# Performance work log

Hardware: AMD Instinct MI355X
Metric: run time of the kernel (lower is better)

Reference implementation:

```python
import jax, jax.numpy as jnp
import numpy as np

NUM_CLASSES = 80
REG_MAX = 16
CLS_W, BOX_W, DFL_W = 1.0, 2.5, 0.5


def _make_anchors(img=640, strides=(8, 16, 32)):
    pts, strs = [], []
    for s in strides:
        n = img // s
        xs = (np.arange(n, dtype=np.float32) + 0.5) * s
        gy, gx = np.meshgrid(xs, xs, indexing='ij')
        pts.append(np.stack([gx.ravel(), gy.ravel()], axis=1))
        strs.append(np.full((n * n, 1), float(s), np.float32))
    return np.concatenate(pts, 0).astype(np.float32), np.concatenate(strs, 0)


def setup_inputs() -> dict:
    key = jax.random.key(0)
    k1, k2, k3, k4, k5 = jax.random.split(key, 5)
    B, G = 16, 20
    ap, st = _make_anchors()  # A = 8400
    A = ap.shape[0]
    cls_scores = jax.random.uniform(k1, (B, A, NUM_CLASSES), dtype=jnp.float32)
    reg_distri = jax.random.normal(k2, (B, A, 4 * (REG_MAX + 1)), dtype=jnp.float32)
    cxcy = jax.random.uniform(k3, (B, G, 2), dtype=jnp.float32) * 560.0 + 40.0
    wh = jax.random.uniform(k4, (B, G, 2), dtype=jnp.float32) * 120.0 + 20.0
    gt_boxes = jnp.concatenate([cxcy - wh * 0.5, cxcy + wh * 0.5], axis=-1)  # xyxy
    gt_labels = jax.random.randint(k5, (B, G), 0, NUM_CLASSES)
    return {"cls_scores": cls_scores, "reg_distri": reg_distri, "gt_boxes": gt_boxes,
            "anchor_points": jnp.asarray(ap), "stride_tensor": jnp.asarray(st),
            "gt_labels": gt_labels}


def _per_image(pred_cls, pred_reg, gt_boxes, gt_labels, anchor_points, stride):
    A, C = pred_cls.shape
    G = gt_boxes.shape[0]
    k = max(min(13, A // max(G, 1)), 3)
    p = jnp.clip(pred_cls, 1e-7, 1.0 - 1e-7)
    centers = (gt_boxes[:, :2] + gt_boxes[:, 2:]) * 0.5                    # [G,2]
    d = jnp.sqrt(jnp.sum((anchor_points[:, None, :] - centers[None]) ** 2, -1))  # [A,G]
    _, topk_idx = jax.lax.top_k(-d.T, k)                                    # [G,k] nearest anchors
    ax = anchor_points[topk_idx]                                            # [G,k,2]
    inside = ((ax[..., 0] >= gt_boxes[:, None, 0]) & (ax[..., 0] <= gt_boxes[:, None, 2]) &
              (ax[..., 1] >= gt_boxes[:, None, 1]) & (ax[..., 1] <= gt_boxes[:, None, 3]))
    any_in = inside.any(-1, keepdims=True)
    assign_k = jnp.where(any_in, inside, jnp.arange(k) < 3)                 # fallback: 3 nearest
    assign = jnp.zeros((G, A), bool).at[jnp.arange(G)[:, None], topk_idx].set(assign_k)
    aT = assign.T                                                           # [A,G]
    fg = aT.any(1)                                                          # [A]
    last_gt = (G - 1) - jnp.argmax(aT[:, ::-1], axis=1)
    target_box = jnp.where(fg[:, None], gt_boxes[last_gt], 0.0)             # [A,4]
    onehot = jax.nn.one_hot(gt_labels, C, dtype=p.dtype)                    # [G,C]
    target_cls = jnp.max(aT[:, :, None].astype(p.dtype) * onehot[None], axis=1)  # [A,C]
    bce = -(target_cls * jnp.log(p) + (1.0 - target_cls) * jnp.log(1.0 - p))
    num_pos = fg.sum().astype(p.dtype)
    pos_w = jnp.minimum(A / jnp.maximum(num_pos, 1.0), 50.0)
    fgf = fg.astype(p.dtype)[:, None]
    pos_loss = jnp.where(num_pos > 0,
                         jnp.sum(bce * fgf) / jnp.maximum(num_pos * C, 1.0) * pos_w, 0.0)
    neg_loss = jnp.sum(bce * (1.0 - fgf)) / jnp.maximum((A - num_pos) * C, 1.0)
    # box decode (DFL expectation) + smooth-L1 on fg anchors
    reg = jax.nn.softmax(pred_reg.reshape(A, 4, REG_MAX + 1), axis=-1)
    proj = jnp.arange(REG_MAX + 1, dtype=p.dtype)
    dist = jnp.sum(reg * proj, axis=-1)                                     # [A,4]
    s = stride[:, 0]
    pb = jnp.stack([anchor_points[:, 0] - dist[:, 0] * s,
                    anchor_points[:, 1] - dist[:, 1] * s,
                    anchor_points[:, 0] + dist[:, 2] * s,
                    anchor_points[:, 1] + dist[:, 3] * s], axis=-1)
    diff = pb - target_box
    ad = jnp.abs(diff)
    sl1 = jnp.where(ad < 1.0, 0.5 * diff * diff, ad - 0.5)
    box_loss = jnp.where(num_pos > 0,
                         jnp.sum(sl1 * fgf) / jnp.maximum(num_pos * 4.0, 1.0), 0.0)
    return pos_loss + neg_loss, box_loss


def reference(cls_scores, reg_distri, gt_boxes, anchor_points, stride_tensor, gt_labels):
    cls_l, box_l = jax.vmap(
        lambda pc, pr, gb, gl: _per_image(pc, pr, gb, gl, anchor_points, stride_tensor)
    )(cls_scores, reg_distri, gt_boxes, gt_labels)
    loss_cls = cls_l.mean() * CLS_W
    loss_box = box_l.mean() * BOX_W
    return loss_cls + loss_box  # loss_dfl is identically 0 in the original
```

## Files before the change

### kernel.cpp

```cpp
#include <hip/hip_runtime.h>
#include <hip/hip_bf16.h>
#include <cfloat>

#define C_NUM 80
#define REG_MAXP1 17
#define NS 33
#define MAXA 8448
#define FG_STRIDE 512

__device__ inline void cand_for_slot(int sc, float cx, float cy, float& v, int& idx)
{
    v = FLT_MAX; idx = 0x7fffffff;
    int loc, w, n, strd, base;
    if (sc < 36)      { loc = sc;      w = 6; n = 80; strd = 8;  base = 0; }
    else if (sc < 52) { loc = sc - 36; w = 4; n = 40; strd = 16; base = 6400; }
    else if (sc < 68) { loc = sc - 52; w = 4; n = 20; strd = 32; base = 8000; }
    else return;
    float inv = 1.0f / (float)strd;
    int ix0 = (int)floorf(cx * inv - 0.5f) - (w / 2 - 1);
    int iy0 = (int)floorf(cy * inv - 0.5f) - (w / 2 - 1);
    int ix = ix0 + loc % w, iy = iy0 + loc / w;
    if (ix < 0 || ix >= n || iy < 0 || iy >= n) return;
    float ax = ((float)ix + 0.5f) * (float)strd;
    float ay = ((float)iy + 0.5f) * (float)strd;
    float dx = ax - cx, dy = ay - cy;
    v = dx * dx + dy * dy;
    idx = base + iy * n + ix;
}

__global__ __launch_bounds__(1024) void assignraster_kernel(const float* __restrict__ gt_boxes,
                              unsigned int* __restrict__ mask,
                              int* __restrict__ fglist,
                              int* __restrict__ npos,
                              float* __restrict__ acc,
                              int A, int G, int k)
{
    __shared__ unsigned int lmask[8400];
    __shared__ int s_cnt;
    int b = blockIdx.x, t = threadIdx.x;
    int wv = t >> 6, lane = t & 63;

    for (int i = t; i < A; i += 1024) lmask[i] = 0u;
    if (t == 0) s_cnt = 0;
    if (t < 3) acc[b * 3 + t] = 0.f;
    __syncthreads();

    for (int g = wv; g < G; g += 16) {
        const float* box = gt_boxes + (size_t)(b * G + g) * 4;
        float x0 = box[0], y0 = box[1], x1 = box[2], y1 = box[3];
        float cx = (x0 + x1) * 0.5f, cy = (y0 + y1) * 0.5f;

        float v0, v1; int i0, i1;
        cand_for_slot(lane,      cx, cy, v0, i0);
        cand_for_slot(lane + 64, cx, cy, v1, i1);

        int my_sel = 0x7fffffff;
        for (int it = 0; it < k; ++it) {
            float lb; int li; bool s0;
            if (v0 < v1 || (v0 == v1 && i0 < i1)) { lb = v0; li = i0; s0 = true; }
            else                                   { lb = v1; li = i1; s0 = false; }
            float rb = lb; int ri = li;
            for (int off = 32; off; off >>= 1) {
                float ov = __shfl_down(rb, off);
                int   oi = __shfl_down(ri, off);
                if (ov < rb || (ov == rb && oi < ri)) { rb = ov; ri = oi; }
            }
            int win = __shfl(ri, 0);
            if (lane == it) my_sel = win;
            if (li == win) {
                if (s0) { v0 = FLT_MAX; i0 = 0x7fffffff; }
                else    { v1 = FLT_MAX; i1 = 0x7fffffff; }
            }
        }

        bool inside = false;
        if (lane < k && my_sel < 0x7fffffff) {
            int idx = my_sel, n, strd, base;
            if (idx < 6400)      { n = 80; strd = 8;  base = 0; }
            else if (idx < 8000) { n = 40; strd = 16; base = 6400; }
            else                 { n = 20; strd = 32; base = 8000; }
            int loc = idx - base;
            float ax = ((float)(loc % n) + 0.5f) * (float)strd;
            float ay = ((float)(loc / n) + 0.5f) * (float)strd;
            inside = (ax >= x0) && (ax <= x1) && (ay >= y0) && (ay <= y1);
        }
        unsigned long long ball = __ballot(inside);
        if (lane < k && my_sel < 0x7fffffff) {
            bool asg = ball ? inside : (lane < 3);
            if (asg) atomicOr(&lmask[my_sel], 1u << g);
        }
    }
    __syncthreads();

    for (int i = t; i < A; i += 1024) {
        unsigned int m = lmask[i];
        mask[(size_t)b * A + i] = m;
        bool fg = (m != 0u);
        unsigned long long bal = __ballot(fg);
        int cnt = __popcll(bal);
        int base = 0;
        if (lane == 0 && cnt) base = atomicAdd(&s_cnt, cnt);
        base = __shfl(base, 0);
        if (fg) {
            int pre = __popcll(bal & ((1ull << lane) - 1ull));
            fglist[b * FG_STRIDE + base + pre] = i | ((31 - __clz(m)) << 16);
        }
    }
    __syncthreads();
    if (t == 0) npos[b] = s_cnt;
}

__global__ __launch_bounds__(256) void assign_kernel(const float* __restrict__ gt_boxes,
                              const float* __restrict__ anchor_points,
                              int* __restrict__ sel,
                              int B, int A, int G, int k)
{
    __shared__ float s_val[4];
    __shared__ int   s_idx[4];
    __shared__ int   s_sel;
    __shared__ int   s_topk[16];
    __shared__ int   s_anyin;

    int bg = blockIdx.x;
    int b = bg / G, g = bg % G;
    const float* box = gt_boxes + (size_t)(b * G + g) * 4;
    float x0 = box[0], y0 = box[1], x1 = box[2], y1 = box[3];
    float cx = (x0 + x1) * 0.5f, cy = (y0 + y1) * 0.5f;

    int t = threadIdx.x;
    float dv[NS];
#pragma unroll
    for (int s = 0; s < NS; ++s) {
        int i = t + s * 256;
        float d = FLT_MAX;
        if (i < A) {
            float dx = anchor_points[2 * i] - cx;
            float dy = anchor_points[2 * i + 1] - cy;
            d = dx * dx + dy * dy;
        }
        dv[s] = d;
    }

    int wid = t >> 6, lane = t & 63;
    for (int it = 0; it < k; ++it) {
        float best = FLT_MAX; int bi = 0x7fffffff;
#pragma unroll
        for (int s = 0; s < NS; ++s) {
            if (dv[s] < best) { best = dv[s]; bi = t + s * 256; }
        }
        for (int off = 32; off; off >>= 1) {
            float ov = __shfl_down(best, off);
            int   oi = __shfl_down(bi, off);
            if (ov < best || (ov == best && oi < bi)) { best = ov; bi = oi; }
        }
        if (lane == 0) { s_val[wid] = best; s_idx[wid] = bi; }
        __syncthreads();
        if (t == 0) {
            float bv = s_val[0]; int bix = s_idx[0];
#pragma unroll
            for (int w = 1; w < 4; ++w) {
                if (s_val[w] < bv || (s_val[w] == bv && s_idx[w] < bix)) { bv = s_val[w]; bix = s_idx[w]; }
            }
            s_sel = bix;
            s_topk[it] = bix;
        }
        __syncthreads();
        int selx = s_sel;
        if ((selx & 255) == t) {
            int slot = selx >> 8;
#pragma unroll
            for (int s = 0; s < NS; ++s) if (s == slot) dv[s] = FLT_MAX;
        }
    }

    if (t == 0) s_anyin = 0;
    __syncthreads();
    bool inside = false; int aidx = -1;
    if (t < k) {
        aidx = s_topk[t];
        float ax = anchor_points[2 * aidx], ay = anchor_points[2 * aidx + 1];
        inside = (ax >= x0) && (ax <= x1) && (ay >= y0) && (ay <= y1);
        if (inside) atomicOr(&s_anyin, 1);
    }
    __syncthreads();
    if (t < k) {
        bool asg = s_anyin ? inside : (t < 3);
        sel[(size_t)bg * 16 + t] = asg ? aidx : -1;
    }
}

__global__ __launch_bounds__(256) void raster_kernel(const int* __restrict__ sel,
                              unsigned int* __restrict__ mask,
                              int* __restrict__ fglist,
                              int* __restrict__ npos,
                              float* __restrict__ acc,
                              int A, int G, int k)
{
    __shared__ unsigned int lmask[MAXA];
    __shared__ int s_cnt;
    int b = blockIdx.x, t = threadIdx.x;

    for (int i = t; i < A; i += 256) lmask[i] = 0u;
    if (t == 0) s_cnt = 0;
    if (t < 3) acc[b * 3 + t] = 0.f;
    __syncthreads();

    for (int i = t; i < G * 16; i += 256) {
        int slot = i & 15;
        if (slot < k) {
            int a = sel[(size_t)(b * G) * 16 + i];
            if (a >= 0) atomicOr(&lmask[a], 1u << (i >> 4));
        }
    }
    __syncthreads();

    for (int i = t; i < A; i += 256) {
        unsigned int m = lmask[i];
        mask[(size_t)b * A + i] = m;
        if (m) {
            int lg = 31 - __clz(m);
            int p = atomicAdd(&s_cnt, 1);
            fglist[b * FG_STRIDE + p] = i | (lg << 16);
        }
    }
    __syncthreads();
    if (t == 0) npos[b] = s_cnt;
}

__device__ inline void bce4(float4 v, unsigned int m, const int* __restrict__ lab,
                            int c0, float& pos, float& neg)
{
    float p0 = fminf(fmaxf(v.x, 1e-7f), 1.0f - 1e-7f);
    float p1 = fminf(fmaxf(v.y, 1e-7f), 1.0f - 1e-7f);
    float p2 = fminf(fmaxf(v.z, 1e-7f), 1.0f - 1e-7f);
    float p3 = fminf(fmaxf(v.w, 1e-7f), 1.0f - 1e-7f);
    if (m) {
        unsigned int tm = 0, mm = m;
        while (mm) {
            int g = __ffs(mm) - 1;
            mm &= mm - 1;
            unsigned int d = (unsigned int)(lab[g] - c0);
            if (d < 4u) tm |= 1u << d;
        }
        pos -= __logf((tm & 1u) ? p0 : 1.0f - p0);
        pos -= __logf((tm & 2u) ? p1 : 1.0f - p1);
        pos -= __logf((tm & 4u) ? p2 : 1.0f - p2);
        pos -= __logf((tm & 8u) ? p3 : 1.0f - p3);
    } else {
        neg -= __logf(1.0f - p0) + __logf(1.0f - p1) + __logf(1.0f - p2) + __logf(1.0f - p3);
    }
}

__global__ __launch_bounds__(256) void cls_kernel(const float4* __restrict__ cls,
                           const unsigned int* __restrict__ mask,
                           const int* __restrict__ gt_labels,
                           float* __restrict__ acc, int A, int G)
{
    const int CQ = C_NUM / 4;
    int b = blockIdx.y;
    int nq = A * CQ;
    const float4* base = cls + (size_t)b * nq;
    const unsigned int* mrow = mask + (size_t)b * A;
    const int* lab = gt_labels + (size_t)b * G;
    int stride = gridDim.x * 256;

    float pos = 0.f, neg = 0.f;
    for (int q0 = blockIdx.x * 256 + threadIdx.x; q0 < nq; q0 += 2 * stride) {
        int q1 = q0 + stride;
        bool h1 = q1 < nq;
        float4 va = base[q0];
        unsigned int ma = mrow[q0 / CQ];
        float4 vb; unsigned int mb = 0;
        if (h1) { vb = base[q1]; mb = mrow[q1 / CQ]; }
        bce4(va, ma, lab, (q0 % CQ) * 4, pos, neg);
        if (h1) bce4(vb, mb, lab, (q1 % CQ) * 4, pos, neg);
    }

    for (int off = 32; off; off >>= 1) {
        pos += __shfl_down(pos, off);
        neg += __shfl_down(neg, off);
    }
    __shared__ float sp[4], sn[4];
    int wid = threadIdx.x >> 6, lane = threadIdx.x & 63;
    if (lane == 0) { sp[wid] = pos; sn[wid] = neg; }
    __syncthreads();
    if (threadIdx.x == 0) {
        float P = sp[0] + sp[1] + sp[2] + sp[3];
        float N = sn[0] + sn[1] + sn[2] + sn[3];
        if (P != 0.f) atomicAdd(&acc[b * 3 + 0], P);
        if (N != 0.f) atomicAdd(&acc[b * 3 + 1], N);
    }
}

__global__ __launch_bounds__(256) void boxfg_kernel(const float* __restrict__ reg,
                           const float* __restrict__ gt_boxes,
                           const float* __restrict__ ap,
                           const float* __restrict__ st,
                           const int* __restrict__ fglist,
                           const int* __restrict__ npos,
                           float* __restrict__ acc, int A, int G)
{
    int b = blockIdx.y;
    int idx = blockIdx.x * 256 + threadIdx.x;
    int e = idx >> 2, j = idx & 3;
    float bx = 0.f;
    if (e < npos[b]) {
        int ent = fglist[b * FG_STRIDE + e];
        int a = ent & 0xffff;
        int lg = ent >> 16;
        float tbj = gt_boxes[(size_t)(b * G + lg) * 4 + j];
        const float* rj = reg + ((size_t)b * A + a) * (4 * REG_MAXP1) + j * REG_MAXP1;
        float rr[REG_MAXP1];
#pragma unroll
        for (int i = 0; i < REG_MAXP1; ++i) rr[i] = rj[i];
        float mx = rr[0];
#pragma unroll
        for (int i = 1; i < REG_MAXP1; ++i) mx = fmaxf(mx, rr[i]);
        float sum = 0.f, dot = 0.f;
#pragma unroll
        for (int i = 0; i < REG_MAXP1; ++i) {
            float ev = __expf(rr[i] - mx);
            sum += ev; dot += ev * (float)i;
        }
        float dist = dot / sum;
        float s = st[a];
        float ac = ap[2 * a + (j & 1)];
        float pbj = (j < 2) ? (ac - dist * s) : (ac + dist * s);
        float df = pbj - tbj;
        float ad = fabsf(df);
        bx = (ad < 1.0f) ? 0.5f * df * df : ad - 0.5f;
    }
    for (int off = 32; off; off >>= 1) bx += __shfl_down(bx, off);
    __shared__ float sb[4];
    int wid = threadIdx.x >> 6, lane = threadIdx.x & 63;
    if (lane == 0) sb[wid] = bx;
    __syncthreads();
    if (threadIdx.x == 0) {
        float X = sb[0] + sb[1] + sb[2] + sb[3];
        if (X != 0.f) atomicAdd(&acc[b * 3 + 2], X);
    }
}

__global__ void final_kernel(const float* __restrict__ acc,
                             const int* __restrict__ npos,
                             float* __restrict__ out, int B, int A)
{
    if (threadIdx.x == 0 && blockIdx.x == 0) {
        float cls_sum = 0.f, box_sum = 0.f;
        for (int b = 0; b < B; ++b) {
            float np = (float)npos[b];
            float neg = acc[b * 3 + 1] / fmaxf(((float)A - np) * (float)C_NUM, 1.0f);
            float pos = 0.f, box = 0.f;
            if (np > 0.f) {
                float pw = fminf((float)A / fmaxf(np, 1.0f), 50.0f);
                pos = acc[b * 3 + 0] / fmaxf(np * (float)C_NUM, 1.0f) * pw;
                box = acc[b * 3 + 2] / fmaxf(np * 4.0f, 1.0f);
            }
            cls_sum += pos + neg;
            box_sum += box;
        }
        out[0] = cls_sum / (float)B * 1.0f + box_sum / (float)B * 2.5f;
    }
}

extern "C" void kernel_launch(void* const* d_in, const int* in_sizes, int n_in,
                              void* d_out, int out_size, void* d_ws, size_t ws_size,
                              hipStream_t stream)
{
    const float* cls   = (const float*)d_in[0];
    const float* reg   = (const float*)d_in[1];
    const float* gtb   = (const float*)d_in[2];
    const float* ap    = (const float*)d_in[3];
    const float* st    = (const float*)d_in[4];
    const int*   glab  = (const int*)d_in[5];

    int A = in_sizes[3] / 2;
    int B = in_sizes[0] / (A * C_NUM);
    int G = in_sizes[5] / B;
    int k = A / (G > 1 ? G : 1); if (k > 13) k = 13; if (k < 3) k = 3;

    unsigned int* mask = (unsigned int*)d_ws;
    float* acc   = (float*)(mask + (size_t)B * A);
    int*   npos  = (int*)(acc + 3 * B);
    int*   sel   = npos + B;
    int*   fgl   = sel + (size_t)B * G * 16;

    if (A == 8400 && G <= 32) {
        assignraster_kernel<<<B, 1024, 0, stream>>>(gtb, mask, fgl, npos, acc, A, G, k);
    } else {
        assign_kernel<<<B * G, 256, 0, stream>>>(gtb, ap, sel, B, A, G, k);
        raster_kernel<<<B, 256, 0, stream>>>(sel, mask, fgl, npos, acc, A, G, k);
    }

    dim3 g3(128, B);
    cls_kernel<<<g3, 256, 0, stream>>>((const float4*)cls, mask, glab, acc, A, G);

    dim3 g4((FG_STRIDE * 4 + 255) / 256, B);
    boxfg_kernel<<<g4, 256, 0, stream>>>(reg, gtb, ap, st, fgl, npos, acc, A, G);

    final_kernel<<<1, 64, 0, stream>>>(acc, npos, (float*)d_out, B, A);
}
```

Baseline: 154.8 us.

## Stream negative BCE unconditionally and fix up foreground anchors in fused kernel

The classification pass now computes the negative BCE term for every element without reading the assignment mask. A separate kernel then subtracts the negative term and adds the positive term for foreground anchors only, and also computes the box loss. The final reduction runs in the last block to finish, using a global counter, which removes the separate final kernel launch. This trades branch-free streaming for an extra correction pass and float cancellation when subtracting terms.

```diff
diff --git a/kernel.cpp b/kernel.cpp
--- a/kernel.cpp
+++ b/kernel.cpp
@@ -3,10 +3,13 @@
 #include <cfloat>
 
 #define C_NUM 80
+#define CQ 20
 #define REG_MAXP1 17
 #define NS 33
 #define MAXA 8448
 #define FG_STRIDE 512
+#define FIX_SLOTS (FG_STRIDE * CQ)
+#define FG_BLOCKS 48
 
 __device__ inline void cand_for_slot(int sc, float cx, float cy, float& v, int& idx)
 {
@@ -33,6 +36,7 @@
                               int* __restrict__ fglist,
                               int* __restrict__ npos,
                               float* __restrict__ acc,
+                              unsigned int* __restrict__ counter,
                               int A, int G, int k)
 {
     __shared__ unsigned int lmask[8400];
@@ -43,6 +47,7 @@
     for (int i = t; i < A; i += 1024) lmask[i] = 0u;
     if (t == 0) s_cnt = 0;
     if (t < 3) acc[b * 3 + t] = 0.f;
+    if (b == 0 && t == 0) *counter = 0u;
     __syncthreads();
 
     for (int g = wv; g < G; g += 16) {
@@ -194,6 +199,7 @@
                               int* __restrict__ fglist,
                               int* __restrict__ npos,
                               float* __restrict__ acc,
+                              unsigned int* __restrict__ counter,
                               int A, int G, int k)
 {
     __shared__ unsigned int lmask[MAXA];
@@ -203,6 +209,7 @@
     for (int i = t; i < A; i += 256) lmask[i] = 0u;
     if (t == 0) s_cnt = 0;
     if (t < 3) acc[b * 3 + t] = 0.f;
+    if (b == 0 && t == 0) *counter = 0u;
     __syncthreads();
 
     for (int i = t; i < G * 16; i += 256) {
@@ -227,139 +234,158 @@
     if (t == 0) npos[b] = s_cnt;
 }
 
-__device__ inline void bce4(float4 v, unsigned int m, const int* __restrict__ lab,
-                            int c0, float& pos, float& neg)
-{
-    float p0 = fminf(fmaxf(v.x, 1e-7f), 1.0f - 1e-7f);
-    float p1 = fminf(fmaxf(v.y, 1e-7f), 1.0f - 1e-7f);
-    float p2 = fminf(fmaxf(v.z, 1e-7f), 1.0f - 1e-7f);
-    float p3 = fminf(fmaxf(v.w, 1e-7f), 1.0f - 1e-7f);
-    if (m) {
-        unsigned int tm = 0, mm = m;
-        while (mm) {
-            int g = __ffs(mm) - 1;
-            mm &= mm - 1;
-            unsigned int d = (unsigned int)(lab[g] - c0);
-            if (d < 4u) tm |= 1u << d;
-        }
-        pos -= __logf((tm & 1u) ? p0 : 1.0f - p0);
-        pos -= __logf((tm & 2u) ? p1 : 1.0f - p1);
-        pos -= __logf((tm & 4u) ? p2 : 1.0f - p2);
-        pos -= __logf((tm & 8u) ? p3 : 1.0f - p3);
-    } else {
+__global__ __launch_bounds__(256) void cls_stream_kernel(const float4* __restrict__ cls,
+                           float* __restrict__ acc, int nq)
+{
+    int b = blockIdx.y;
+    const float4* base = cls + (size_t)b * nq;
+    int stride = gridDim.x * 256;
+    float neg = 0.f;
+    for (int q = blockIdx.x * 256 + threadIdx.x; q < nq; q += stride) {
+        float4 v = base[q];
+        float p0 = fminf(fmaxf(v.x, 1e-7f), 1.0f - 1e-7f);
+        float p1 = fminf(fmaxf(v.y, 1e-7f), 1.0f - 1e-7f);
+        float p2 = fminf(fmaxf(v.z, 1e-7f), 1.0f - 1e-7f);
+        float p3 = fminf(fmaxf(v.w, 1e-7f), 1.0f - 1e-7f);
         neg -= __logf(1.0f - p0) + __logf(1.0f - p1) + __logf(1.0f - p2) + __logf(1.0f - p3);
     }
-}
-
-__global__ __launch_bounds__(256) void cls_kernel(const float4* __restrict__ cls,
+    for (int off = 32; off; off >>= 1) neg += __shfl_down(neg, off);
+    __shared__ float sn[4];
+    int wid = threadIdx.x >> 6, lane = threadIdx.x & 63;
+    if (lane == 0) sn[wid] = neg;
+    __syncthreads();
+    if (threadIdx.x == 0) {
+        float N = sn[0] + sn[1] + sn[2] + sn[3];
+        atomicAdd(&acc[b * 3 + 1], N);
+    }
+}
+
+__global__ __launch_bounds__(256) void fgfix_kernel(const float4* __restrict__ cls4,
+                           const float* __restrict__ reg,
+                           const float* __restrict__ gt_boxes,
+                           const float* __restrict__ ap,
+                           const float* __restrict__ st,
                            const unsigned int* __restrict__ mask,
                            const int* __restrict__ gt_labels,
-                           float* __restrict__ acc, int A, int G)
-{
-    const int CQ = C_NUM / 4;
+                           const int* __restrict__ fglist,
+                           const int* __restrict__ npos,
+                           float* __restrict__ acc,
+                           unsigned int* __restrict__ counter,
+                           float* __restrict__ out,
+                           int A, int G, int B)
+{
     int b = blockIdx.y;
-    int nq = A * CQ;
-    const float4* base = cls + (size_t)b * nq;
-    const unsigned int* mrow = mask + (size_t)b * A;
-    const int* lab = gt_labels + (size_t)b * G;
-    int stride = gridDim.x * 256;
-
-    float pos = 0.f, neg = 0.f;
-    for (int q0 = blockIdx.x * 256 + threadIdx.x; q0 < nq; q0 += 2 * stride) {
-        int q1 = q0 + stride;
-        bool h1 = q1 < nq;
-        float4 va = base[q0];
-        unsigned int ma = mrow[q0 / CQ];
-        float4 vb; unsigned int mb = 0;
-        if (h1) { vb = base[q1]; mb = mrow[q1 / CQ]; }
-        bce4(va, ma, lab, (q0 % CQ) * 4, pos, neg);
-        if (h1) bce4(vb, mb, lab, (q1 % CQ) * 4, pos, neg);
+    int idx = blockIdx.x * 256 + threadIdx.x;
+    int np = npos[b];
+    float posAdd = 0.f, negSub = 0.f, bx = 0.f;
+
+    if (idx < FIX_SLOTS) {
+        int e = idx / CQ, cq = idx - e * CQ;
+        if (e < np) {
+            int ent = fglist[b * FG_STRIDE + e];
+            int a = ent & 0xffff;
+            unsigned int m = mask[(size_t)b * A + a];
+            const int* lab = gt_labels + (size_t)b * G;
+            int c0 = cq * 4;
+            float4 v = cls4[(size_t)b * A * CQ + (size_t)a * CQ + cq];
+            float p0 = fminf(fmaxf(v.x, 1e-7f), 1.0f - 1e-7f);
+            float p1 = fminf(fmaxf(v.y, 1e-7f), 1.0f - 1e-7f);
+            float p2 = fminf(fmaxf(v.z, 1e-7f), 1.0f - 1e-7f);
+            float p3 = fminf(fmaxf(v.w, 1e-7f), 1.0f - 1e-7f);
+            unsigned int tm = 0, mm = m;
+            while (mm) {
+                int g = __ffs(mm) - 1;
+                mm &= mm - 1;
+                unsigned int d = (unsigned int)(lab[g] - c0);
+                if (d < 4u) tm |= 1u << d;
+            }
+            float n0 = -__logf(1.0f - p0), n1 = -__logf(1.0f - p1);
+            float n2 = -__logf(1.0f - p2), n3 = -__logf(1.0f - p3);
+            negSub = n0 + n1 + n2 + n3;
+            posAdd  = (tm & 1u) ? -__logf(p0) : n0;
+            posAdd += (tm & 2u) ? -__logf(p1) : n1;
+            posAdd += (tm & 4u) ? -__logf(p2) : n2;
+            posAdd += (tm & 8u) ? -__logf(p3) : n3;
+        }
+    } else {
+        int idx2 = idx - FIX_SLOTS;
+        int e = idx2 >> 2, j = idx2 & 3;
+        if (e < np) {
+            int ent = fglist[b * FG_STRIDE + e];
+            int a = ent & 0xffff;
+            int lg = ent >> 16;
+            float tbj = gt_boxes[(size_t)(b * G + lg) * 4 + j];
+            const float* rj = reg + ((size_t)b * A + a) * (4 * REG_MAXP1) + j * REG_MAXP1;
+            float rr[REG_MAXP1];
+#pragma unroll
+            for (int i = 0; i < REG_MAXP1; ++i) rr[i] = rj[i];
+            float mx = rr[0];
+#pragma unroll
+            for (int i = 1; i < REG_MAXP1; ++i) mx = fmaxf(mx, rr[i]);
+            float sum = 0.f, dot = 0.f;
+#pragma unroll
+            for (int i = 0; i < REG_MAXP1; ++i) {
+                float ev = __expf(rr[i] - mx);
+                sum += ev; dot += ev * (float)i;
+            }
+            float dist = dot / sum;
+            float s = st[a];
+            float ac = ap[2 * a + (j & 1)];
+            float pbj = (j < 2) ? (ac - dist * s) : (ac + dist * s);
+            float df = pbj - tbj;
+            float ad = fabsf(df);
+            bx = (ad < 1.0f) ? 0.5f * df * df : ad - 0.5f;
+        }
     }
 
     for (int off = 32; off; off >>= 1) {
-        pos += __shfl_down(pos, off);
-        neg += __shfl_down(neg, off);
-    }
-    __shared__ float sp[4], sn[4];
+        posAdd += __shfl_down(posAdd, off);
+        negSub += __shfl_down(negSub, off);
+        bx     += __shfl_down(bx, off);
+    }
+    __shared__ float sp[4], sn[4], sb[4];
+    __shared__ int s_last;
     int wid = threadIdx.x >> 6, lane = threadIdx.x & 63;
-    if (lane == 0) { sp[wid] = pos; sn[wid] = neg; }
+    if (lane == 0) { sp[wid] = posAdd; sn[wid] = negSub; sb[wid] = bx; }
     __syncthreads();
     if (threadIdx.x == 0) {
         float P = sp[0] + sp[1] + sp[2] + sp[3];
         float N = sn[0] + sn[1] + sn[2] + sn[3];
+        float X = sb[0] + sb[1] + sb[2] + sb[3];
         if (P != 0.f) atomicAdd(&acc[b * 3 + 0], P);
-        if (N != 0.f) atomicAdd(&acc[b * 3 + 1], N);
-    }
-}
-
-__global__ __launch_bounds__(256) void boxfg_kernel(const float* __restrict__ reg,
-                           const float* __restrict__ gt_boxes,
-                           const float* __restrict__ ap,
-                           const float* __restrict__ st,
-                           const int* __restrict__ fglist,
-                           const int* __restrict__ npos,
-                           float* __restrict__ acc, int A, int G)
-{
-    int b = blockIdx.y;
-    int idx = blockIdx.x * 256 + threadIdx.x;
-    int e = idx >> 2, j = idx & 3;
-    float bx = 0.f;
-    if (e < npos[b]) {
-        int ent = fglist[b * FG_STRIDE + e];
-        int a = ent & 0xffff;
-        int lg = ent >> 16;
-        float tbj = gt_boxes[(size_t)(b * G + lg) * 4 + j];
-        const float* rj = reg + ((size_t)b * A + a) * (4 * REG_MAXP1) + j * REG_MAXP1;
-        float rr[REG_MAXP1];
-#pragma unroll
-        for (int i = 0; i < REG_MAXP1; ++i) rr[i] = rj[i];
-        float mx = rr[0];
-#pragma unroll
-        for (int i = 1; i < REG_MAXP1; ++i) mx = fmaxf(mx, rr[i]);
-        float sum = 0.f, dot = 0.f;
-#pragma unroll
-        for (int i = 0; i < REG_MAXP1; ++i) {
-            float ev = __expf(rr[i] - mx);
-            sum += ev; dot += ev * (float)i;
-        }
-        float dist = dot / sum;
-        float s = st[a];
-        float ac = ap[2 * a + (j & 1)];
-        float pbj = (j < 2) ? (ac - dist * s) : (ac + dist * s);
-        float df = pbj - tbj;
-        float ad = fabsf(df);
-        bx = (ad < 1.0f) ? 0.5f * df * df : ad - 0.5f;
-    }
-    for (int off = 32; off; off >>= 1) bx += __shfl_down(bx, off);
-    __shared__ float sb[4];
-    int wid = threadIdx.x >> 6, lane = threadIdx.x & 63;
-    if (lane == 0) sb[wid] = bx;
-    __syncthreads();
-    if (threadIdx.x == 0) {
-        float X = sb[0] + sb[1] + sb[2] + sb[3];
+        if (N != 0.f) atomicAdd(&acc[b * 3 + 1], -N);
         if (X != 0.f) atomicAdd(&acc[b * 3 + 2], X);
-    }
-}
-
-__global__ void final_kernel(const float* __restrict__ acc,
-                             const int* __restrict__ npos,
-                             float* __restrict__ out, int B, int A)
-{
-    if (threadIdx.x == 0 && blockIdx.x == 0) {
-        float cls_sum = 0.f, box_sum = 0.f;
-        for (int b = 0; b < B; ++b) {
-            float np = (float)npos[b];
-            float neg = acc[b * 3 + 1] / fmaxf(((float)A - np) * (float)C_NUM, 1.0f);
-            float pos = 0.f, box = 0.f;
-            if (np > 0.f) {
-                float pw = fminf((float)A / fmaxf(np, 1.0f), 50.0f);
-                pos = acc[b * 3 + 0] / fmaxf(np * (float)C_NUM, 1.0f) * pw;
-                box = acc[b * 3 + 2] / fmaxf(np * 4.0f, 1.0f);
-            }
-            cls_sum += pos + neg;
-            box_sum += box;
-        }
-        out[0] = cls_sum / (float)B * 1.0f + box_sum / (float)B * 2.5f;
+        __threadfence();
+        unsigned int old = atomicAdd(counter, 1u);
+        s_last = (old == (unsigned int)(gridDim.x * gridDim.y) - 1u) ? 1 : 0;
+    }
+    __syncthreads();
+
+    if (s_last) {
+        int t = threadIdx.x;
+        float cls_c = 0.f, box_c = 0.f;
+        if (t < 64) {
+            for (int bb = t; bb < B; bb += 64) {
+                float a0 = atomicAdd(&acc[bb * 3 + 0], 0.f);
+                float a1 = atomicAdd(&acc[bb * 3 + 1], 0.f);
+                float a2 = atomicAdd(&acc[bb * 3 + 2], 0.f);
+                float npf = (float)npos[bb];
+                float neg = a1 / fmaxf(((float)A - npf) * (float)C_NUM, 1.0f);
+                float pos = 0.f, box = 0.f;
+                if (npf > 0.f) {
+                    float pw = fminf((float)A / fmaxf(npf, 1.0f), 50.0f);
+                    pos = a0 / fmaxf(npf * (float)C_NUM, 1.0f) * pw;
+                    box = a2 / fmaxf(npf * 4.0f, 1.0f);
+                }
+                cls_c += pos + neg;
+                box_c += box;
+            }
+            for (int off = 32; off; off >>= 1) {
+                cls_c += __shfl_down(cls_c, off);
+                box_c += __shfl_down(box_c, off);
+            }
+            if (t == 0) out[0] = cls_c / (float)B * 1.0f + box_c / (float)B * 2.5f;
+        }
     }
 }
 
@@ -384,19 +410,20 @@
     int*   npos  = (int*)(acc + 3 * B);
     int*   sel   = npos + B;
     int*   fgl   = sel + (size_t)B * G * 16;
+    unsigned int* counter = (unsigned int*)(fgl + (size_t)B * FG_STRIDE);
 
     if (A == 8400 && G <= 32) {
-        assignraster_kernel<<<B, 1024, 0, stream>>>(gtb, mask, fgl, npos, acc, A, G, k);
+        assignraster_kernel<<<B, 1024, 0, stream>>>(gtb, mask, fgl, npos, acc, counter, A, G, k);
     } else {
         assign_kernel<<<B * G, 256, 0, stream>>>(gtb, ap, sel, B, A, G, k);
-        raster_kernel<<<B, 256, 0, stream>>>(sel, mask, fgl, npos, acc, A, G, k);
+        raster_kernel<<<B, 256, 0, stream>>>(sel, mask, fgl, npos, acc, counter, A, G, k);
     }
 
     dim3 g3(128, B);
-    cls_kernel<<<g3, 256, 0, stream>>>((const float4*)cls, mask, glab, acc, A, G);
-
-    dim3 g4((FG_STRIDE * 4 + 255) / 256, B);
-    boxfg_kernel<<<g4, 256, 0, stream>>>(reg, gtb, ap, st, fgl, npos, acc, A, G);
-
-    final_kernel<<<1, 64, 0, stream>>>(acc, npos, (float*)d_out, B, A);
-}
+    cls_stream_kernel<<<g3, 256, 0, stream>>>((const float4*)cls, acc, A * CQ);
+
+    dim3 g4(FG_BLOCKS, B);
+    fgfix_kernel<<<g4, 256, 0, stream>>>((const float4*)cls, reg, gtb, ap, st,
+                                         mask, glab, fgl, npos, acc, counter,
+                                         (float*)d_out, A, G, B);
+}
```

Result: no change. 153.6 us (-0.8%).
